# Optimization experiments

Hardware: AMD Instinct MI355X
Metric: run time of the kernel (lower is better)

The kernel has to match this reference:

```python
import jax, jax.numpy as jnp
import numpy as np

B, T, H, L, V = 16, 512, 512, 2, 32000

def setup_inputs() -> dict:
    key = jax.random.key(0)
    k1, k2, k3, k4 = jax.random.split(key, 4)
    tokens = jax.random.randint(k1, (B, T), 0, V)
    embed = jax.random.normal(k2, (V, H), dtype=jnp.float32) * 0.02
    W = jax.random.normal(k3, (L, 2 * H, 4 * H), dtype=jnp.float32) * (1.0 / np.sqrt(2 * H))
    b = jnp.zeros((L, 4 * H), dtype=jnp.float32)
    Wout = jax.random.normal(k4, (H, V), dtype=jnp.float32) * (1.0 / np.sqrt(H))
    bout = jnp.zeros((V,), dtype=jnp.float32)
    return {"tokens": tokens, "embed": embed, "W": W, "b": b, "Wout": Wout, "bout": bout}

def _run_layer(h_seq, Wl, bl):
    # h_seq: [T, B, H]
    hid = Wl.shape[1] // 4
    def step(carry, x_t):
        c, h = carry
        gates = jnp.concatenate([x_t, h], axis=-1) @ Wl + bl  # [B, 4H]
        i, f, g, o = jnp.split(gates, 4, axis=-1)
        i = jax.nn.sigmoid(i)
        f = jax.nn.sigmoid(f)
        g = jnp.tanh(g)
        o = jax.nn.sigmoid(o)
        new_c = f * c + i * g
        new_h = o * jnp.tanh(new_c)
        return (new_c, new_h), new_h
    Bsz = h_seq.shape[1]
    init = (jnp.zeros((Bsz, hid), h_seq.dtype), jnp.zeros((Bsz, hid), h_seq.dtype))
    _, out = jax.lax.scan(step, init, h_seq)
    return out  # [T, B, H]

def reference(tokens, embed, W, b, Wout, bout):
    h = embed[tokens]                     # [B, T, H]
    h = jnp.transpose(h, (1, 0, 2))       # [T, B, H] for scan
    for l in range(W.shape[0]):
        h = _run_layer(h, W[l], b[l])
    h = jnp.transpose(h, (1, 0, 2))       # [B, T, H]
    logits = h @ Wout + bout              # [B, T, V]
    return logits
```

## Files before the change

kernel.cpp:

```cpp
#include <hip/hip_runtime.h>
#include <stdint.h>

#define Tn 512
#define Hn 512
#define Vn 32000
#define KIN 1024
#define G4 2048
#define NBLK 256
#define PHASES 513
#define PSTR 40
#define XSTR 1032
#define SLOT_STRIDE 2048

typedef __attribute__((ext_vector_type(8))) short short8;
typedef __attribute__((ext_vector_type(4))) float f32x4;
typedef __attribute__((ext_vector_type(4))) int i32x4;
typedef __attribute__((ext_vector_type(4))) unsigned u32x4;

__device__ __forceinline__ unsigned short f2bf(float v) {
  unsigned int x = __float_as_uint(v);
  return (unsigned short)((x + 0x7fffu + ((x >> 16) & 1u)) >> 16);
}
__device__ __forceinline__ float bf2f(unsigned short u) {
  return __uint_as_float(((unsigned int)u) << 16);
}
__device__ __forceinline__ unsigned pollld(const unsigned* p) {
  return __hip_atomic_load(p, __ATOMIC_RELAXED, __HIP_MEMORY_SCOPE_AGENT);
}
__device__ __forceinline__ void flagst(unsigned* p, unsigned v) {
  __hip_atomic_store(p, v, __ATOMIC_RELAXED, __HIP_MEMORY_SCOPE_AGENT);
}

__device__ __forceinline__ void ld4x4_sc1(const unsigned* p0, const unsigned* p1,
                                          const unsigned* p2, const unsigned* p3,
                                          u32x4& a, u32x4& b, u32x4& c, u32x4& d) {
  asm volatile(
      "global_load_dwordx4 %0, %4, off sc1\n\t"
      "global_load_dwordx4 %1, %5, off sc1\n\t"
      "global_load_dwordx4 %2, %6, off sc1\n\t"
      "global_load_dwordx4 %3, %7, off sc1\n\t"
      "s_waitcnt vmcnt(0)"
      : "=&v"(a), "=&v"(b), "=&v"(c), "=&v"(d)
      : "v"(p0), "v"(p1), "v"(p2), "v"(p3)
      : "memory");
}
__device__ __forceinline__ void ld8x4_sc1(
    const unsigned* p0, const unsigned* p1, const unsigned* p2, const unsigned* p3,
    const unsigned* p4, const unsigned* p5, const unsigned* p6, const unsigned* p7,
    u32x4& a, u32x4& b, u32x4& c, u32x4& d,
    u32x4& e, u32x4& f, u32x4& g, u32x4& h) {
  asm volatile(
      "global_load_dwordx4 %0, %8, off sc1\n\t"
      "global_load_dwordx4 %1, %9, off sc1\n\t"
      "global_load_dwordx4 %2, %10, off sc1\n\t"
      "global_load_dwordx4 %3, %11, off sc1\n\t"
      "global_load_dwordx4 %4, %12, off sc1\n\t"
      "global_load_dwordx4 %5, %13, off sc1\n\t"
      "global_load_dwordx4 %6, %14, off sc1\n\t"
      "global_load_dwordx4 %7, %15, off sc1\n\t"
      "s_waitcnt vmcnt(0)"
      : "=&v"(a), "=&v"(b), "=&v"(c), "=&v"(d),
        "=&v"(e), "=&v"(f), "=&v"(g), "=&v"(h)
      : "v"(p0), "v"(p1), "v"(p2), "v"(p3),
        "v"(p4), "v"(p5), "v"(p6), "v"(p7)
      : "memory");
}

__device__ __forceinline__ void unpack8(const u32x4& a, const u32x4& b,
                                        unsigned short* XhDst, unsigned short* XlDst) {
  unsigned hw[4], lw[4];
  hw[0] = (a[0] >> 16) | (a[1] & 0xffff0000u);
  lw[0] = (a[0] & 0xffffu) | (a[1] << 16);
  hw[1] = (a[2] >> 16) | (a[3] & 0xffff0000u);
  lw[1] = (a[2] & 0xffffu) | (a[3] << 16);
  hw[2] = (b[0] >> 16) | (b[1] & 0xffff0000u);
  lw[2] = (b[0] & 0xffffu) | (b[1] << 16);
  hw[3] = (b[2] >> 16) | (b[3] & 0xffff0000u);
  lw[3] = (b[2] & 0xffffu) | (b[3] << 16);
  *(u32x4*)XhDst = *(const u32x4*)hw;
  *(u32x4*)XlDst = *(const u32x4*)lw;
}

__device__ __forceinline__ void cvt8(const f32x4& v0, const f32x4& v1,
                                     unsigned short* XhDst, unsigned short* XlDst) {
  unsigned short h8[8], l8[8];
#pragma unroll
  for (int i = 0; i < 4; ++i) {
    h8[i]     = f2bf(v0[i]); l8[i]     = f2bf(v0[i] - bf2f(h8[i]));
    h8[4 + i] = f2bf(v1[i]); l8[4 + i] = f2bf(v1[i] - bf2f(h8[4 + i]));
  }
  *(u32x4*)XhDst = *(const u32x4*)h8;
  *(u32x4*)XlDst = *(const u32x4*)l8;
}

__global__ __launch_bounds__(256) void wout_convert(const float* __restrict__ Wout,
                                                    unsigned short* __restrict__ BhT,
                                                    unsigned short* __restrict__ BlT) {
  __shared__ float ts[64][65];
  const int n0 = blockIdx.x * 64;
  const int k0 = blockIdx.y * 64;
  const int tid = threadIdx.x;
  {
    const int c = tid & 63, rq = tid >> 6;
#pragma unroll
    for (int i = 0; i < 16; ++i) {
      const int k = rq * 16 + i;
      ts[k][c] = Wout[(size_t)(k0 + k) * Vn + (n0 + c)];
    }
  }
  __syncthreads();
  {
    const int nl = tid >> 2;
    const int ks = (tid & 3) * 16;
    unsigned short hb[16], lb[16];
#pragma unroll
    for (int i = 0; i < 16; ++i) {
      const float v = ts[ks + i][nl];
      const unsigned short h = f2bf(v);
      hb[i] = h;
      lb[i] = f2bf(v - bf2f(h));
    }
    const size_t base = (size_t)(n0 + nl) * Hn + (k0 + ks);
    *(i32x4*)&BhT[base]     = *(const i32x4*)&hb[0];
    *(i32x4*)&BhT[base + 8] = *(const i32x4*)&hb[8];
    *(i32x4*)&BlT[base]     = *(const i32x4*)&lb[0];
    *(i32x4*)&BlT[base + 8] = *(const i32x4*)&lb[8];
  }
}

__global__ __launch_bounds__(512) void lstm_scan(
    const int* __restrict__ tokens, const float* __restrict__ embed,
    const float* __restrict__ Wg, const float* __restrict__ bg,
    unsigned* __restrict__ hex1, unsigned* __restrict__ hex2,
    unsigned short* __restrict__ Ah, unsigned short* __restrict__ Al,
    unsigned* __restrict__ arr) {

  extern __shared__ char smembytes[];
  unsigned short* Wh  = (unsigned short*)smembytes;
  unsigned short* Wlo = Wh + 16 * XSTR;
  unsigned short* Xh  = Wlo + 16 * XSTR;
  unsigned short* Xl  = Xh + 16 * XSTR;
  float* red   = (float*)(Xl + 16 * XSTR);
  float* gates = red + 8 * 272;

  const int tid = threadIdx.x;
  const int bid = blockIdx.x;
  const int layer = bid >> 7;
  const int u0 = (bid & 127) * 4;

  for (int idx = tid; idx < 16 * KIN; idx += 512) {
    const int k = idx >> 4;
    const int c = idx & 15;
    const int col = ((c >> 2) << 9) + u0 + (c & 3);
    const float wv = Wg[(size_t)layer * KIN * G4 + (size_t)k * G4 + col];
    const unsigned short h = f2bf(wv);
    Wh[c * XSTR + k] = h;
    Wlo[c * XSTR + k] = f2bf(wv - bf2f(h));
  }

  float bb0 = 0.f, bb1 = 0.f, bb2 = 0.f, bb3 = 0.f, c_state = 0.f;
  if (tid < 64) {
    const int j = tid & 3;
    bb0 = bg[layer * G4 + 0 * 512 + u0 + j];
    bb1 = bg[layer * G4 + 1 * 512 + u0 + j];
    bb2 = bg[layer * G4 + 2 * 512 + u0 + j];
    bb3 = bg[layer * G4 + 3 * 512 + u0 + j];
  }

  const int lane = tid & 63;
  const int w = tid >> 6;
  const int m = lane & 15;
  const int g8 = (lane >> 4) * 8;

  const int gA = tid, gB = tid + 512;
  const int rowA = gA >> 6, slotA = gA & 63;
  const int rowB = gB >> 6, slotB = gB & 63;
  const int offA = rowA * XSTR + slotA * 8;
  const int offB = rowB * XSTR + slotB * 8;

  unsigned* bar_my = (unsigned*)((char*)arr + (size_t)bid * SLOT_STRIDE);
  const unsigned* bar_poll =
      (const unsigned*)((const char*)arr + (size_t)(tid & 255) * SLOT_STRIDE);

  __syncthreads();

  short8 wh_r[4], wl_r[4];
#pragma unroll
  for (int it = 0; it < 4; ++it) {
    const int kb = w * 128 + it * 32 + g8;
    wh_r[it] = *(const short8*)&Wh[m * XSTR + kb];
    wl_r[it] = *(const short8*)&Wlo[m * XSTR + kb];
  }

  if (layer == 0) {
    const int tokA = tokens[rowA * Tn + 0];
    const int tokB = tokens[rowB * Tn + 0];
    const float* sA = embed + (size_t)tokA * Hn + slotA * 8;
    const float* sB = embed + (size_t)tokB * Hn + slotB * 8;
    cvt8(*(const f32x4*)sA, *(const f32x4*)(sA + 4), &Xh[offA], &Xl[offA]);
    cvt8(*(const f32x4*)sB, *(const f32x4*)(sB + 4), &Xh[offB], &Xl[offB]);
  }

  for (int ph = 0; ph < PHASES; ++ph) {
    const unsigned target = (unsigned)(ph + 1);
    const bool act = (layer == 0) ? (ph < Tn) : (ph >= 1);

    if (act) {
      if (layer == 0) {
        const unsigned* hb = hex1 + ((ph - 1) & 1) * 8192;
        u32x4 a, b, c, d;
        ld4x4_sc1(hb + gA * 8, hb + gA * 8 + 4, hb + gB * 8, hb + gB * 8 + 4,
                  a, b, c, d);
        unpack8(a, b, &Xh[offA + 512], &Xl[offA + 512]);
        unpack8(c, d, &Xh[offB + 512], &Xl[offB + 512]);
      } else {
        const unsigned* xb = hex1 + ((ph - 1) & 1) * 8192;
        const unsigned* hb = hex2 + (ph & 1) * 8192;
        u32x4 x0, x1, x2, x3, h0, h1v, h2v, h3;
        ld8x4_sc1(xb + gA * 8, xb + gA * 8 + 4, xb + gB * 8, xb + gB * 8 + 4,
                  hb + gA * 8, hb + gA * 8 + 4, hb + gB * 8, hb + gB * 8 + 4,
                  x0, x1, x2, x3, h0, h1v, h2v, h3);
        unpack8(x0, x1, &Xh[offA], &Xl[offA]);
        unpack8(x2, x3, &Xh[offB], &Xl[offB]);
        unpack8(h0, h1v, &Xh[offA + 512], &Xl[offA + 512]);
        unpack8(h2v, h3, &Xh[offB + 512], &Xl[offB + 512]);
      }
    }
    __syncthreads();

    if (act) {
      f32x4 acc = {0.f, 0.f, 0.f, 0.f};
#pragma unroll
      for (int it = 0; it < 4; ++it) {
        const int kb = w * 128 + it * 32 + g8;
        const short8 ahf = *(const short8*)&Xh[m * XSTR + kb];
        const short8 alf = *(const short8*)&Xl[m * XSTR + kb];
        acc = __builtin_amdgcn_mfma_f32_16x16x32_bf16(ahf, wh_r[it], acc, 0, 0, 0);
        acc = __builtin_amdgcn_mfma_f32_16x16x32_bf16(ahf, wl_r[it], acc, 0, 0, 0);
        acc = __builtin_amdgcn_mfma_f32_16x16x32_bf16(alf, wh_r[it], acc, 0, 0, 0);
      }
      const int r0 = (lane >> 4) * 4;
#pragma unroll
      for (int r = 0; r < 4; ++r)
        red[w * 272 + (r0 + r) * 17 + m] = acc[r];
    }
    __syncthreads();

    if (act && tid < 256) {
      const int b = tid >> 4, c = tid & 15;
      float s = 0.f;
#pragma unroll
      for (int ww = 0; ww < 8; ++ww) s += red[ww * 272 + b * 17 + c];
      gates[tid] = s;
    }
    __syncthreads();

    if (act && tid < 64) {
      const int b = tid >> 2, j = tid & 3;
      const float gi = gates[b * 16 + j] + bb0;
      const float gf = gates[b * 16 + 4 + j] + bb1;
      const float gg = gates[b * 16 + 8 + j] + bb2;
      const float go = gates[b * 16 + 12 + j] + bb3;
      const float si = 1.f / (1.f + __expf(-gi));
      const float sf = 1.f / (1.f + __expf(-gf));
      const float e2g = __expf(2.f * gg);
      const float tg = 1.f - 2.f / (e2g + 1.f);
      const float so = 1.f / (1.f + __expf(-go));
      const float cn = sf * c_state + si * tg;
      c_state = cn;
      const float e2c = __expf(2.f * cn);
      const float hn = so * (1.f - 2.f / (e2c + 1.f));
      const unsigned short hh = f2bf(hn);
      const unsigned short hl = f2bf(hn - bf2f(hh));
      const unsigned pk = ((unsigned)hh << 16) | (unsigned)hl;
      unsigned* hdst = (layer == 0)
          ? hex1 + (ph & 1) * 8192 + b * 512 + (u0 + j)
          : hex2 + ((ph - 1) & 1) * 8192 + b * 512 + (u0 + j);
      flagst(hdst, pk);
      if (layer == 1) {
        const size_t r = (size_t)(ph - 1) * 16 + b;
        Ah[r * Hn + u0 + j] = hh;
        Al[r * Hn + u0 + j] = hl;
      }
    }
    __syncthreads();

    if (tid == 0) flagst(bar_my, target);

    if (layer == 0 && (ph + 1) < Tn) {
      const int t1 = ph + 1;
      const int tokA = tokens[rowA * Tn + t1];
      const int tokB = tokens[rowB * Tn + t1];
      const float* sA = embed + (size_t)tokA * Hn + slotA * 8;
      const float* sB = embed + (size_t)tokB * Hn + slotB * 8;
      cvt8(*(const f32x4*)sA, *(const f32x4*)(sA + 4), &Xh[offA], &Xl[offA]);
      cvt8(*(const f32x4*)sB, *(const f32x4*)(sB + 4), &Xh[offB], &Xl[offB]);
    }

    if (tid < 256) {
      while (pollld(bar_poll) < target) __builtin_amdgcn_s_sleep(2);
    }
    __syncthreads();
  }
}

__global__ __launch_bounds__(256) void proj_gemm(
    const unsigned short* __restrict__ Ah_, const unsigned short* __restrict__ Al_,
    const unsigned short* __restrict__ Bh_, const unsigned short* __restrict__ Bl_,
    const float* __restrict__ bout, float* __restrict__ out) {
  __shared__ unsigned short sAh[128 * PSTR], sAl[128 * PSTR], sBh[128 * PSTR], sBl[128 * PSTR];
  const int tid = threadIdx.x;
  const int n0 = blockIdx.x * 128;
  const int m0 = blockIdx.y * 128;
  const int lane = tid & 63, w = tid >> 6;
  const int wm = (w & 1) * 64, wn = (w >> 1) * 64;

  f32x4 acc[4][4];
#pragma unroll
  for (int i = 0; i < 4; ++i)
#pragma unroll
    for (int j = 0; j < 4; ++j) acc[i][j] = (f32x4){0.f, 0.f, 0.f, 0.f};

  for (int kt = 0; kt < 16; ++kt) {
    const int k0 = kt * 32;
    __syncthreads();
#pragma unroll
    for (int i = 0; i < 8; ++i) {
      const int chunk = ((i & 1) << 8) + tid;
      const int mrow = chunk >> 2;
      const int kc = chunk & 3;
      const int tsel = i >> 1;
      const unsigned short* gsrc =
          (tsel == 0) ? Ah_ + (size_t)(m0 + mrow) * Hn + k0 + kc * 8 :
          (tsel == 1) ? Al_ + (size_t)(m0 + mrow) * Hn + k0 + kc * 8 :
          (tsel == 2) ? Bh_ + (size_t)(n0 + mrow) * Hn + k0 + kc * 8 :
                        Bl_ + (size_t)(n0 + mrow) * Hn + k0 + kc * 8;
      unsigned short* ldst = (tsel == 0) ? sAh : (tsel == 1) ? sAl : (tsel == 2) ? sBh : sBl;
      *(i32x4*)&ldst[mrow * PSTR + kc * 8] = *(const i32x4*)gsrc;
    }
    __syncthreads();

    short8 fah[4], fal[4], fbh[4], fbl[4];
    const int rlo = lane & 15, kg = (lane >> 4) * 8;
#pragma unroll
    for (int f = 0; f < 4; ++f) {
      fah[f] = *(const short8*)&sAh[(wm + f * 16 + rlo) * PSTR + kg];
      fal[f] = *(const short8*)&sAl[(wm + f * 16 + rlo) * PSTR + kg];
      fbh[f] = *(const short8*)&sBh[(wn + f * 16 + rlo) * PSTR + kg];
      fbl[f] = *(const short8*)&sBl[(wn + f * 16 + rlo) * PSTR + kg];
    }
#pragma unroll
    for (int i = 0; i < 4; ++i)
#pragma unroll
      for (int j = 0; j < 4; ++j) {
        acc[i][j] = __builtin_amdgcn_mfma_f32_16x16x32_bf16(fah[i], fbh[j], acc[i][j], 0, 0, 0);
        acc[i][j] = __builtin_amdgcn_mfma_f32_16x16x32_bf16(fah[i], fbl[j], acc[i][j], 0, 0, 0);
        acc[i][j] = __builtin_amdgcn_mfma_f32_16x16x32_bf16(fal[i], fbh[j], acc[i][j], 0, 0, 0);
      }
  }

#pragma unroll
  for (int j = 0; j < 4; ++j) {
    const int n = n0 + wn + j * 16 + (lane & 15);
    const float bv = bout[n];
#pragma unroll
    for (int i = 0; i < 4; ++i) {
#pragma unroll
      for (int r = 0; r < 4; ++r) {
        const int m = m0 + wm + i * 16 + ((lane >> 4) * 4) + r;
        out[(size_t)(m & 15) * ((size_t)Tn * Vn) + (size_t)(m >> 4) * Vn + n] =
            acc[i][j][r] + bv;
      }
    }
  }
}

extern "C" void kernel_launch(void* const* d_in, const int* in_sizes, int n_in,
                              void* d_out, int out_size, void* d_ws, size_t ws_size,
                              hipStream_t stream) {
  const int*   tokens = (const int*)d_in[0];
  const float* embed  = (const float*)d_in[1];
  const float* W      = (const float*)d_in[2];
  const float* bias   = (const float*)d_in[3];
  const float* Wout   = (const float*)d_in[4];
  const float* bout   = (const float*)d_in[5];
  float* out = (float*)d_out;

  char* ws = (char*)d_ws;
  unsigned* arr  = (unsigned*)ws;
  unsigned* hex1 = (unsigned*)(ws + 524288);
  unsigned* hex2 = (unsigned*)(ws + 524288 + 65536);
  unsigned short* Ah  = (unsigned short*)(ws + 655360);
  unsigned short* Al  = Ah + (size_t)8192 * 512;
  unsigned short* BhT = Al + (size_t)8192 * 512;
  unsigned short* BlT = BhT + (size_t)32000 * 512;

  hipMemsetAsync(d_ws, 0, 655360, stream);

  wout_convert<<<dim3(500, 8), 256, 0, stream>>>(Wout, BhT, BlT);

  const size_t ldsbytes = (size_t)(4 * 16 * XSTR) * 2 +
                          (size_t)(8 * 272 + 256) * 4;
  (void)hipFuncSetAttribute((const void*)lstm_scan,
                            hipFuncAttributeMaxDynamicSharedMemorySize, (int)ldsbytes);
  lstm_scan<<<NBLK, 512, ldsbytes, stream>>>(tokens, embed, W, bias,
                                             hex1, hex2, Ah, Al, arr);

  proj_gemm<<<dim3(250, 64), 256, 0, stream>>>(Ah, Al, BhT, BlT, bout, out);
}
```

Before: 2.795 ms.

## Fuse gate reduction into activation step, drop barriers, swizzle projection grid

The per-step cross-wave reduction now runs inside the 64 activation threads instead of a separate 256-thread pass, which removes one __syncthreads and the gates buffer. A block-wide barrier before publishing the step flag is replaced by a vmcnt wait in the first wave only, shortening the critical path of each recurrent step. The projection GEMM moves to a 1D grid with a swizzled tile order that groups M tiles so B tiles can be reused in L2. The risk is ordering: LDS reuse of red across steps now relies on the remaining barriers, and the flag is published without a full block barrier.

```diff
diff --git a/kernel.cpp b/kernel.cpp
--- a/kernel.cpp
+++ b/kernel.cpp
@@ -140,8 +140,7 @@
   unsigned short* Wlo = Wh + 16 * XSTR;
   unsigned short* Xh  = Wlo + 16 * XSTR;
   unsigned short* Xl  = Xh + 16 * XSTR;
-  float* red   = (float*)(Xl + 16 * XSTR);
-  float* gates = red + 8 * 272;
+  float* red = (float*)(Xl + 16 * XSTR);
 
   const int tid = threadIdx.x;
   const int bid = blockIdx.x;
@@ -246,21 +245,21 @@
     }
     __syncthreads();
 
-    if (act && tid < 256) {
-      const int b = tid >> 4, c = tid & 15;
-      float s = 0.f;
-#pragma unroll
-      for (int ww = 0; ww < 8; ++ww) s += red[ww * 272 + b * 17 + c];
-      gates[tid] = s;
-    }
-    __syncthreads();
-
     if (act && tid < 64) {
       const int b = tid >> 2, j = tid & 3;
-      const float gi = gates[b * 16 + j] + bb0;
-      const float gf = gates[b * 16 + 4 + j] + bb1;
-      const float gg = gates[b * 16 + 8 + j] + bb2;
-      const float go = gates[b * 16 + 12 + j] + bb3;
+      float g4[4];
+#pragma unroll
+      for (int g = 0; g < 4; ++g) {
+        const int c = g * 4 + j;
+        float s = 0.f;
+#pragma unroll
+        for (int ww = 0; ww < 8; ++ww) s += red[ww * 272 + b * 17 + c];
+        g4[g] = s;
+      }
+      const float gi = g4[0] + bb0;
+      const float gf = g4[1] + bb1;
+      const float gg = g4[2] + bb2;
+      const float go = g4[3] + bb3;
       const float si = 1.f / (1.f + __expf(-gi));
       const float sf = 1.f / (1.f + __expf(-gf));
       const float e2g = __expf(2.f * gg);
@@ -283,9 +282,10 @@
         Al[r * Hn + u0 + j] = hl;
       }
     }
-    __syncthreads();
-
-    if (tid == 0) flagst(bar_my, target);
+    if (tid < 64) {
+      asm volatile("s_waitcnt vmcnt(0)" ::: "memory");
+      if (tid == 0) flagst(bar_my, target);
+    }
 
     if (layer == 0 && (ph + 1) < Tn) {
       const int t1 = ph + 1;
@@ -310,8 +310,10 @@
     const float* __restrict__ bout, float* __restrict__ out) {
   __shared__ unsigned short sAh[128 * PSTR], sAl[128 * PSTR], sBh[128 * PSTR], sBl[128 * PSTR];
   const int tid = threadIdx.x;
-  const int n0 = blockIdx.x * 128;
-  const int m0 = blockIdx.y * 128;
+  const int id = blockIdx.x;
+  const int mt = (id & 7) * 8 + ((id >> 3) & 7);
+  const int m0 = mt * 128;
+  const int n0 = (id >> 6) * 128;
   const int lane = tid & 63, w = tid >> 6;
   const int wm = (w & 1) * 64, wn = (w >> 1) * 64;
 
@@ -399,12 +401,11 @@
 
   wout_convert<<<dim3(500, 8), 256, 0, stream>>>(Wout, BhT, BlT);
 
-  const size_t ldsbytes = (size_t)(4 * 16 * XSTR) * 2 +
-                          (size_t)(8 * 272 + 256) * 4;
+  const size_t ldsbytes = (size_t)(4 * 16 * XSTR) * 2 + (size_t)(8 * 272) * 4;
   (void)hipFuncSetAttribute((const void*)lstm_scan,
                             hipFuncAttributeMaxDynamicSharedMemorySize, (int)ldsbytes);
   lstm_scan<<<NBLK, 512, ldsbytes, stream>>>(tokens, embed, W, bias,
                                              hex1, hex2, Ah, Al, arr);
 
-  proj_gemm<<<dim3(250, 64), 256, 0, stream>>>(Ah, Al, BhT, BlT, bout, out);
-}
+  proj_gemm<<<16000, 256, 0, stream>>>(Ah, Al, BhT, BlT, bout, out);
+}
```

Result: slower. 3.266 ms (+16.9%).
